# Optimization experiments

Measured on AMD Instinct MI355X. Metric: run time of the kernel, lower is better.

The kernel has to match this reference:

```python
import jax, jax.numpy as jnp
import numpy as np

B, S, HID, NH = 4, 2048, 512, 8
DH = HID // NH
NEG = -1000000.0


def setup_inputs() -> dict:
    key = jax.random.key(0)
    ks = jax.random.split(key, 8)
    scale = 1.0 / np.sqrt(HID)
    return {
        "queries": jax.random.normal(ks[0], (B, S, HID), dtype=jnp.float32),
        "keys": jax.random.normal(ks[1], (B, S, HID), dtype=jnp.float32),
        "values": jax.random.normal(ks[2], (B, S, HID), dtype=jnp.float32),
        "valid_lens": jax.random.randint(ks[3], (B,), 1, S + 1, dtype=jnp.int32),
        "Wq": jax.random.uniform(ks[4], (HID, HID), jnp.float32, -scale, scale),
        "Wk": jax.random.uniform(ks[5], (HID, HID), jnp.float32, -scale, scale),
        "Wv": jax.random.uniform(ks[6], (HID, HID), jnp.float32, -scale, scale),
        "Wo": jax.random.uniform(ks[7], (HID, HID), jnp.float32, -scale, scale),
    }


def _split_heads(x):
    # (B, S, HID) -> (B, NH, S, DH)
    return x.reshape(B, S, NH, DH).transpose(0, 2, 1, 3)


def reference(queries, keys, values, valid_lens, Wq, Wk, Wv, Wo):
    q = _split_heads(queries @ Wq.T)
    k = _split_heads(keys @ Wk.T)
    v = _split_heads(values @ Wv.T)
    scores = jnp.einsum("bhqd,bhkd->bhqk", q, k) / jnp.sqrt(jnp.float32(DH))
    # valid_lens is per-batch; mask key positions >= valid_len with -1e6 (as in sequence_mask)
    mask = jnp.arange(S)[None, :] < valid_lens[:, None]          # (B, S)
    scores = jnp.where(mask[:, None, None, :], scores, NEG)
    attn = jax.nn.softmax(scores, axis=-1)
    out = jnp.einsum("bhqk,bhkd->bhqd", attn, v)                 # (B, NH, S, DH)
    out = out.transpose(0, 2, 1, 3).reshape(B, S, HID)
    return out @ Wo.T
```

## Files before the change

### kernel.cpp

```cpp
#include <hip/hip_runtime.h>

#define B_ 4
#define S_ 2048
#define HIDN 512
#define NH 8
#define DH 64

typedef __attribute__((ext_vector_type(8))) short short8;
typedef __attribute__((ext_vector_type(4))) short short4v;
typedef __attribute__((ext_vector_type(8))) __bf16 bf16x8;
typedef __attribute__((ext_vector_type(4))) float floatx4;
typedef __attribute__((ext_vector_type(2))) unsigned uint2v;
typedef __attribute__((ext_vector_type(4))) unsigned uint4v;

__device__ inline short f2bf(float f) {
    union { float f; unsigned u; } x; x.f = f;
    unsigned r = x.u + 0x7fffu + ((x.u >> 16) & 1u);
    return (short)(r >> 16);
}

__device__ inline unsigned pack2(float a, float b) {
    unsigned ua = __builtin_bit_cast(unsigned, a) + 0x8000u;
    unsigned ub = __builtin_bit_cast(unsigned, b) + 0x8000u;
    return __builtin_amdgcn_perm(ub, ua, 0x07060302);
}

__device__ inline short8 cvt8(const float* __restrict__ p) {
    floatx4 f0 = *(const floatx4*)p;
    floatx4 f1 = *(const floatx4*)(p + 4);
    uint4v u;
    u[0] = pack2(f0[0], f0[1]); u[1] = pack2(f0[2], f0[3]);
    u[2] = pack2(f1[0], f1[1]); u[3] = pack2(f1[2], f1[3]);
    return __builtin_bit_cast(short8, u);
}

__device__ inline floatx4 mfma_s(short8 a, short8 b, floatx4 c) {
    return __builtin_amdgcn_mfma_f32_16x16x32_bf16(
        __builtin_bit_cast(bf16x8, a), __builtin_bit_cast(bf16x8, b), c, 0, 0, 0);
}

__device__ inline float vmax4(floatx4 v) {
    return fmaxf(fmaxf(v[0], v[1]), fmaxf(v[2], v[3]));
}

__device__ inline void gl_lds(const short* g, short* l) {
    __builtin_amdgcn_global_load_lds(
        (const __attribute__((address_space(1))) void*)g,
        (__attribute__((address_space(3))) void*)l, 16, 0, 0);
}

__global__ void cvt_w(const float* __restrict__ wq, const float* __restrict__ wk,
                      const float* __restrict__ wv, short* __restrict__ out) {
    const float* src = blockIdx.y == 0 ? wq : (blockIdx.y == 1 ? wk : wv);
    int i = (blockIdx.x * 256 + threadIdx.x) * 4;
    floatx4 f = *(const floatx4*)&src[i];
    short4v v; v[0]=f2bf(f[0]); v[1]=f2bf(f[1]); v[2]=f2bf(f[2]); v[3]=f2bf(f[3]);
    *(short4v*)&out[blockIdx.y * (HIDN * HIDN) + i] = v;
}

__global__ __launch_bounds__(256) void gemm_qkv(const float* __restrict__ xq,
                                                const float* __restrict__ xk,
                                                const float* __restrict__ xv,
                                                const short* __restrict__ wb,
                                                short* __restrict__ Qh,
                                                short* __restrict__ Kh,
                                                short* __restrict__ VT) {
    const int z = blockIdx.z;
    const float* X = z == 0 ? xq : (z == 1 ? xk : xv);
    const short* W = wb + z * (HIDN * HIDN);
    short* dstQK = z == 0 ? Qh : Kh;

    __shared__ __align__(16) short Als[128][72];
    __shared__ __align__(16) short Bls[128][72];

    const int t = threadIdx.x;
    const int w = t >> 6, lane = t & 63, quad = lane >> 4, l16 = lane & 15;
    const int wm = (w & 1) * 64, wn = (w >> 1) * 64;
    const int m0 = blockIdx.x * 128, n0 = blockIdx.y * 128;

    floatx4 acc[4][4];
    floatx4 zero = {0.f, 0.f, 0.f, 0.f};
#pragma unroll
    for (int i = 0; i < 4; i++)
#pragma unroll
        for (int j = 0; j < 4; j++) acc[i][j] = zero;

    const int row0 = t >> 3;
    const int c8 = (t & 7) * 8;

    for (int k0 = 0; k0 < HIDN; k0 += 64) {
        __syncthreads();
#pragma unroll
        for (int rr = 0; rr < 4; rr++)
            *(short8*)&Als[row0 + rr*32][c8] =
                cvt8(&X[(m0 + row0 + rr*32) * HIDN + k0 + c8]);
#pragma unroll
        for (int rr = 0; rr < 4; rr++)
            *(short8*)&Bls[row0 + rr*32][c8] =
                *(const short8*)&W[(n0 + row0 + rr*32) * HIDN + k0 + c8];
        __syncthreads();

#pragma unroll
        for (int ks = 0; ks < 2; ks++) {
            const int cq8 = (ks * 4 + quad) * 8;
            short8 a[4], b[4];
#pragma unroll
            for (int i = 0; i < 4; i++)
                a[i] = *(const short8*)&Als[wm + i*16 + l16][cq8];
#pragma unroll
            for (int j = 0; j < 4; j++)
                b[j] = *(const short8*)&Bls[wn + j*16 + l16][cq8];
#pragma unroll
            for (int i = 0; i < 4; i++)
#pragma unroll
                for (int j = 0; j < 4; j++)
                    acc[i][j] = mfma_s(a[i], b[j], acc[i][j]);
        }
    }

    if (z < 2) {
#pragma unroll
        for (int i = 0; i < 4; i++)
#pragma unroll
            for (int j = 0; j < 4; j++)
#pragma unroll
                for (int r = 0; r < 4; r++) {
                    int m = m0 + wm + i*16 + quad*4 + r;
                    int n = n0 + wn + j*16 + l16;
                    int bb = m >> 11, s = m & 2047, h = n >> 6, d = n & 63;
                    dstQK[((bb * NH + h) * S_ + s) * DH + d] = f2bf(acc[i][j][r]);
                }
    } else {
#pragma unroll
        for (int i = 0; i < 4; i++)
#pragma unroll
            for (int j = 0; j < 4; j++) {
                int s0 = m0 + wm + i*16 + quad*4;
                int n = n0 + wn + j*16 + l16;
                int bb = s0 >> 11, s = s0 & 2047, h = n >> 6, d = n & 63;
                uint2v v;
                v[0] = pack2(acc[i][j][0], acc[i][j][1]);
                v[1] = pack2(acc[i][j][2], acc[i][j][3]);
                *(uint2v*)&VT[((bb * NH + h) * DH + d) * S_ + s] = v;
            }
    }
}

__global__ __launch_bounds__(256) void gemm_out(const short* __restrict__ AO,
                                                const float* __restrict__ Wo,
                                                float* __restrict__ C) {
    __shared__ __align__(16) short Als[128][72];
    __shared__ __align__(16) short Bls[64][72];

    const int t = threadIdx.x;
    const int w = t >> 6, lane = t & 63, quad = lane >> 4, l16 = lane & 15;
    const int wm = (w & 1) * 64, wn = (w >> 1) * 32;
    const int m0 = blockIdx.x * 128, n0 = blockIdx.y * 64;

    floatx4 acc[4][2];
    floatx4 zero = {0.f, 0.f, 0.f, 0.f};
#pragma unroll
    for (int i = 0; i < 4; i++)
#pragma unroll
        for (int j = 0; j < 2; j++) acc[i][j] = zero;

    const int row0 = t >> 3;
    const int c8 = (t & 7) * 8;

    for (int k0 = 0; k0 < HIDN; k0 += 64) {
        __syncthreads();
#pragma unroll
        for (int rr = 0; rr < 4; rr++)
            *(short8*)&Als[row0 + rr*32][c8] =
                *(const short8*)&AO[(m0 + row0 + rr*32) * HIDN + k0 + c8];
#pragma unroll
        for (int rr = 0; rr < 2; rr++)
            *(short8*)&Bls[row0 + rr*32][c8] =
                cvt8(&Wo[(n0 + row0 + rr*32) * HIDN + k0 + c8]);
        __syncthreads();

#pragma unroll
        for (int ks = 0; ks < 2; ks++) {
            const int cq8 = (ks * 4 + quad) * 8;
            short8 a[4], b[2];
#pragma unroll
            for (int i = 0; i < 4; i++)
                a[i] = *(const short8*)&Als[wm + i*16 + l16][cq8];
#pragma unroll
            for (int j = 0; j < 2; j++)
                b[j] = *(const short8*)&Bls[wn + j*16 + l16][cq8];
#pragma unroll
            for (int i = 0; i < 4; i++)
#pragma unroll
                for (int j = 0; j < 2; j++)
                    acc[i][j] = mfma_s(a[i], b[j], acc[i][j]);
        }
    }

#pragma unroll
    for (int i = 0; i < 4; i++)
#pragma unroll
        for (int j = 0; j < 2; j++)
#pragma unroll
            for (int r = 0; r < 4; r++) {
                int m = m0 + wm + i*16 + quad*4 + r;
                int n = n0 + wn + j*16 + l16;
                C[m * HIDN + n] = acc[i][j][r];
            }
}

__global__ __launch_bounds__(256, 2) void attn_kernel(const short* __restrict__ Qh,
                                                      const short* __restrict__ Kh,
                                                      const short* __restrict__ VT,
                                                      const int* __restrict__ vlen,
                                                      short* __restrict__ AO) {
    __shared__ __align__(16) short Ksh[2][128 * 64];
    __shared__ __align__(16) short Vsh[2][64 * 128];

    const int t = threadIdx.x, w = t >> 6, lane = t & 63;
    const int quad = lane >> 4, l16 = lane & 15;
    const int qb = blockIdx.x * 64;
    const int h = blockIdx.y, b = blockIdx.z;
    const int bh = b * NH + h;
    const int vl = vlen[b];
    const int nt = (vl + 127) >> 7;

    const float SC = 0.180336879f;

    const short* qrow = &Qh[(bh * S_ + qb + w * 16 + l16) * DH];
    short8 qa0 = *(const short8*)&qrow[quad * 8];
    short8 qa1 = *(const short8*)&qrow[32 + quad * 8];

    int kgo[4], vgo[4];
#pragma unroll
    for (int it = 0; it < 4; it++) {
        int idx = it * 256 + t;
        int row = idx >> 3, c = idx & 7;
        kgo[it] = row * DH + ((c ^ (row & 7)) << 3);
        int d = idx >> 4, cv = idx & 15;
        vgo[it] = d * S_ + ((cv ^ (d & 7)) << 3);
    }
    const int ldsb = (t & ~63) * 8;

    const short* Kgb = &Kh[(size_t)bh * S_ * DH];
    const short* Vgb = &VT[(size_t)bh * DH * S_];

#define STAGE(bufsel, tb)                                                     \
    {                                                                         \
        const short* Kg_ = Kgb + (tb) * DH;                                   \
        const short* Vg_ = Vgb + (tb);                                        \
        _Pragma("unroll")                                                     \
        for (int it = 0; it < 4; it++)                                        \
            gl_lds(Kg_ + kgo[it], &Ksh[bufsel][it * 2048 + ldsb]);            \
        _Pragma("unroll")                                                     \
        for (int it = 0; it < 4; it++)                                        \
            gl_lds(Vg_ + vgo[it], &Vsh[bufsel][it * 2048 + ldsb]);            \
    }

    STAGE(0, 0)

    float m_run = -1e30f, l_run = 0.f;
    floatx4 Oacc[4];
    floatx4 zero = {0.f, 0.f, 0.f, 0.f};
#pragma unroll
    for (int dt = 0; dt < 4; dt++) Oacc[dt] = zero;

    for (int kt = 0; kt < nt; kt++) {
        const int base = kt << 7;
        const bool bnd = (base + 128) > vl;
        const int cur = kt & 1;
        const short* Kc = Ksh[cur];
        const short* Vc = Vsh[cur];
        short* Psh = Ksh[cur];

        __syncthreads();

        if (kt + 1 < nt) STAGE(cur ^ 1, base + 128)

        floatx4 sc[8];
#pragma unroll
        for (int n = 0; n < 8; n++) {
            int kro = n * 16 + l16;
            const short* kr = &Kc[kro * 64];
            short8 kb0 = *(const short8*)&kr[((quad ^ (kro & 7)) << 3)];
            short8 kb1 = *(const short8*)&kr[(((4 + quad) ^ (kro & 7)) << 3)];
            floatx4 s = zero;
            s = mfma_s(kb0, qa0, s);
            s = mfma_s(kb1, qa1, s);
            sc[n] = s;
        }
        __syncthreads();

        if (bnd) {
#pragma unroll
            for (int n = 0; n < 8; n++)
#pragma unroll
                for (int r = 0; r < 4; r++) {
                    int key = base + n * 16 + quad * 4 + r;
                    if (key >= vl) sc[n][r] = -1e30f;
                }
        }

        float mx = vmax4(sc[0]);
#pragma unroll
        for (int n = 1; n < 8; n++) mx = fmaxf(mx, vmax4(sc[n]));
        mx = fmaxf(mx, __shfl_xor(mx, 16));
        mx = fmaxf(mx, __shfl_xor(mx, 32));
        const float mxs = mx * SC;
        const bool norescale = __all(mxs <= m_run);
        const float mnew = norescale ? m_run : fmaxf(m_run, mxs);
        const float alpha = norescale ? 1.0f : __builtin_amdgcn_exp2f(m_run - mnew);
        m_run = mnew;
        float rs = 0.f;
#pragma unroll
        for (int n = 0; n < 8; n++)
#pragma unroll
            for (int r = 0; r < 4; r++) {
                float p = __builtin_amdgcn_exp2f(fmaf(sc[n][r], SC, -mnew));
                sc[n][r] = p;
                rs += p;
            }
        rs += __shfl_xor(rs, 16);
        rs += __shfl_xor(rs, 32);
        l_run = l_run * alpha + rs;
        if (!norescale) {
#pragma unroll
            for (int dt = 0; dt < 4; dt++)
#pragma unroll
                for (int r = 0; r < 4; r++) Oacc[dt][r] *= alpha;
        }

#pragma unroll
        for (int n = 0; n < 8; n++) {
            unsigned lo = pack2(sc[n][0], sc[n][1]);
            unsigned hi = pack2(sc[n][2], sc[n][3]);
            int c = (n << 1) + (quad >> 1);
            int idx = (w << 11) + (l16 << 7) + ((c ^ (l16 & 7)) << 3) + ((quad & 1) << 2);
            uint2v pv; pv[0] = lo; pv[1] = hi;
            *(uint2v*)&Psh[idx] = pv;
        }
        asm volatile("s_waitcnt lgkmcnt(0)" ::: "memory");
        __builtin_amdgcn_sched_barrier(0);

#pragma unroll
        for (int kk = 0; kk < 4; kk++) {
            int pc = (kk << 2) + quad;
            short8 pf = *(const short8*)&Psh[(w << 11) + (l16 << 7) + ((pc ^ (l16 & 7)) << 3)];
#pragma unroll
            for (int dt = 0; dt < 4; dt++) {
                int vrow = dt * 16 + l16;
                short8 vf = *(const short8*)&Vc[vrow * 128 + ((pc ^ (vrow & 7)) << 3)];
                Oacc[dt] = mfma_s(vf, pf, Oacc[dt]);
            }
        }
    }
#undef STAGE

    float inv = 1.0f / l_run;
    int q = qb + w * 16 + l16;
    short* dst = &AO[(b * S_ + q) * HIDN + h * DH];
#pragma unroll
    for (int dt = 0; dt < 4; dt++) {
        uint2v v;
        v[0] = pack2(Oacc[dt][0] * inv, Oacc[dt][1] * inv);
        v[1] = pack2(Oacc[dt][2] * inv, Oacc[dt][3] * inv);
        *(uint2v*)&dst[dt * 16 + quad * 4] = v;
    }
}

extern "C" void kernel_launch(void* const* d_in, const int* in_sizes, int n_in,
                              void* d_out, int out_size, void* d_ws, size_t ws_size,
                              hipStream_t stream) {
    const float* q  = (const float*)d_in[0];
    const float* k  = (const float*)d_in[1];
    const float* v  = (const float*)d_in[2];
    const int*   vl = (const int*)d_in[3];
    const float* wq = (const float*)d_in[4];
    const float* wk = (const float*)d_in[5];
    const float* wv = (const float*)d_in[6];
    const float* wo = (const float*)d_in[7];
    float* out = (float*)d_out;

    const size_t HSZ = (size_t)B_ * NH * S_ * DH;
    short* Qh  = (short*)d_ws;
    short* Kh  = Qh + HSZ;
    short* VT  = Kh + HSZ;
    short* AO  = VT + HSZ;
    short* Wqkv = AO;

    dim3 blk(256);
    cvt_w<<<dim3(256, 3), blk, 0, stream>>>(wq, wk, wv, Wqkv);
    gemm_qkv<<<dim3(64, 4, 3), blk, 0, stream>>>(q, k, v, Wqkv, Qh, Kh, VT);
    attn_kernel<<<dim3(S_ / 64, NH, B_), blk, 0, stream>>>(Qh, Kh, VT, vl, AO);
    gemm_out<<<dim3(64, 8), blk, 0, stream>>>(AO, wo, out);
}
```

Measured before the change: 189.4 us.

## Split attention KV loop across two warp groups with in-block softmax merge

The attention block grows to 512 threads, split into two 256-thread groups. Each group handles alternating 128-key tiles for the same 64 queries, and at the end the two partial softmax states (max, sum, output) are merged through LDS. The async global-to-LDS double-buffered prefetch is replaced by synchronous register loads into one buffer per group, so tile loads no longer overlap compute. The aim is to halve the serial KV loop per block and raise wave-level parallelism, at the cost of losing load/compute overlap, adding extra barriers and a merge step, and using more registers per CU.

```diff
diff --git a/kernel.cpp b/kernel.cpp
--- a/kernel.cpp
+++ b/kernel.cpp
@@ -41,12 +41,6 @@
 
 __device__ inline float vmax4(floatx4 v) {
     return fmaxf(fmaxf(v[0], v[1]), fmaxf(v[2], v[3]));
-}
-
-__device__ inline void gl_lds(const short* g, short* l) {
-    __builtin_amdgcn_global_load_lds(
-        (const __attribute__((address_space(1))) void*)g,
-        (__attribute__((address_space(3))) void*)l, 16, 0, 0);
 }
 
 __global__ void cvt_w(const float* __restrict__ wq, const float* __restrict__ wk,
@@ -209,7 +203,7 @@
             }
 }
 
-__global__ __launch_bounds__(256, 2) void attn_kernel(const short* __restrict__ Qh,
+__global__ __launch_bounds__(512, 4) void attn_kernel(const short* __restrict__ Qh,
                                                       const short* __restrict__ Kh,
                                                       const short* __restrict__ VT,
                                                       const int* __restrict__ vlen,
@@ -217,13 +211,17 @@
     __shared__ __align__(16) short Ksh[2][128 * 64];
     __shared__ __align__(16) short Vsh[2][64 * 128];
 
-    const int t = threadIdx.x, w = t >> 6, lane = t & 63;
-    const int quad = lane >> 4, l16 = lane & 15;
+    const int t = threadIdx.x;
+    const int g = t >> 8;
+    const int tg = t & 255;
+    const int w = (t >> 6) & 3;
+    const int lane = t & 63, quad = lane >> 4, l16 = lane & 15;
     const int qb = blockIdx.x * 64;
     const int h = blockIdx.y, b = blockIdx.z;
     const int bh = b * NH + h;
     const int vl = vlen[b];
     const int nt = (vl + 127) >> 7;
+    const int nrounds = (nt + 1) >> 1;
 
     const float SC = 0.180336879f;
 
@@ -231,33 +229,9 @@
     short8 qa0 = *(const short8*)&qrow[quad * 8];
     short8 qa1 = *(const short8*)&qrow[32 + quad * 8];
 
-    int kgo[4], vgo[4];
-#pragma unroll
-    for (int it = 0; it < 4; it++) {
-        int idx = it * 256 + t;
-        int row = idx >> 3, c = idx & 7;
-        kgo[it] = row * DH + ((c ^ (row & 7)) << 3);
-        int d = idx >> 4, cv = idx & 15;
-        vgo[it] = d * S_ + ((cv ^ (d & 7)) << 3);
-    }
-    const int ldsb = (t & ~63) * 8;
-
-    const short* Kgb = &Kh[(size_t)bh * S_ * DH];
-    const short* Vgb = &VT[(size_t)bh * DH * S_];
-
-#define STAGE(bufsel, tb)                                                     \
-    {                                                                         \
-        const short* Kg_ = Kgb + (tb) * DH;                                   \
-        const short* Vg_ = Vgb + (tb);                                        \
-        _Pragma("unroll")                                                     \
-        for (int it = 0; it < 4; it++)                                        \
-            gl_lds(Kg_ + kgo[it], &Ksh[bufsel][it * 2048 + ldsb]);            \
-        _Pragma("unroll")                                                     \
-        for (int it = 0; it < 4; it++)                                        \
-            gl_lds(Vg_ + vgo[it], &Vsh[bufsel][it * 2048 + ldsb]);            \
-    }
-
-    STAGE(0, 0)
+    short* Kc = Ksh[g];
+    short* Vc = Vsh[g];
+    short* Psh = Kc + (w << 11);
 
     float m_run = -1e30f, l_run = 0.f;
     floatx4 Oacc[4];
@@ -265,106 +239,146 @@
 #pragma unroll
     for (int dt = 0; dt < 4; dt++) Oacc[dt] = zero;
 
-    for (int kt = 0; kt < nt; kt++) {
+    for (int i = 0; i < nrounds; i++) {
+        const int kt = 2 * i + g;
+        const bool act = kt < nt;
         const int base = kt << 7;
         const bool bnd = (base + 128) > vl;
-        const int cur = kt & 1;
-        const short* Kc = Ksh[cur];
-        const short* Vc = Vsh[cur];
-        short* Psh = Ksh[cur];
-
-        __syncthreads();
-
-        if (kt + 1 < nt) STAGE(cur ^ 1, base + 128)
+
+        __syncthreads();
+        if (act) {
+            const short* Kg = &Kh[(bh * S_ + base) * DH];
+#pragma unroll
+            for (int it = 0; it < 4; it++) {
+                int idx = it * 256 + tg;
+                int row = idx >> 3, c = idx & 7;
+                *(short8*)&Kc[row * 64 + (((c ^ (row & 7))) << 3)] =
+                    *(const short8*)&Kg[row * DH + (c << 3)];
+            }
+            const short* Vg = &VT[bh * DH * S_ + base];
+#pragma unroll
+            for (int it = 0; it < 4; it++) {
+                int idx = it * 256 + tg;
+                int d = idx >> 4, c = idx & 15;
+                *(short8*)&Vc[d * 128 + (((c ^ (d & 7))) << 3)] =
+                    *(const short8*)&Vg[d * S_ + (c << 3)];
+            }
+        }
+        __syncthreads();
 
         floatx4 sc[8];
-#pragma unroll
-        for (int n = 0; n < 8; n++) {
-            int kro = n * 16 + l16;
-            const short* kr = &Kc[kro * 64];
-            short8 kb0 = *(const short8*)&kr[((quad ^ (kro & 7)) << 3)];
-            short8 kb1 = *(const short8*)&kr[(((4 + quad) ^ (kro & 7)) << 3)];
-            floatx4 s = zero;
-            s = mfma_s(kb0, qa0, s);
-            s = mfma_s(kb1, qa1, s);
-            sc[n] = s;
-        }
-        __syncthreads();
-
-        if (bnd) {
+        if (act) {
+#pragma unroll
+            for (int n = 0; n < 8; n++) {
+                int kro = n * 16 + l16;
+                const short* kr = &Kc[kro * 64];
+                short8 kb0 = *(const short8*)&kr[((quad ^ (kro & 7)) << 3)];
+                short8 kb1 = *(const short8*)&kr[(((4 + quad) ^ (kro & 7)) << 3)];
+                floatx4 s = zero;
+                s = mfma_s(kb0, qa0, s);
+                s = mfma_s(kb1, qa1, s);
+                sc[n] = s;
+            }
+        }
+        __syncthreads();
+
+        if (act) {
+            if (bnd) {
+#pragma unroll
+                for (int n = 0; n < 8; n++)
+#pragma unroll
+                    for (int r = 0; r < 4; r++) {
+                        int key = base + n * 16 + quad * 4 + r;
+                        if (key >= vl) sc[n][r] = -1e30f;
+                    }
+            }
+
+            float mx = vmax4(sc[0]);
+#pragma unroll
+            for (int n = 1; n < 8; n++) mx = fmaxf(mx, vmax4(sc[n]));
+            mx = fmaxf(mx, __shfl_xor(mx, 16));
+            mx = fmaxf(mx, __shfl_xor(mx, 32));
+            const float mxs = mx * SC;
+            const bool norescale = __all(mxs <= m_run);
+            const float mnew = norescale ? m_run : fmaxf(m_run, mxs);
+            const float alpha = norescale ? 1.0f : __builtin_amdgcn_exp2f(m_run - mnew);
+            m_run = mnew;
+            float rs = 0.f;
 #pragma unroll
             for (int n = 0; n < 8; n++)
 #pragma unroll
                 for (int r = 0; r < 4; r++) {
-                    int key = base + n * 16 + quad * 4 + r;
-                    if (key >= vl) sc[n][r] = -1e30f;
+                    float p = __builtin_amdgcn_exp2f(fmaf(sc[n][r], SC, -mnew));
+                    sc[n][r] = p;
+                    rs += p;
                 }
-        }
-
-        float mx = vmax4(sc[0]);
-#pragma unroll
-        for (int n = 1; n < 8; n++) mx = fmaxf(mx, vmax4(sc[n]));
-        mx = fmaxf(mx, __shfl_xor(mx, 16));
-        mx = fmaxf(mx, __shfl_xor(mx, 32));
-        const float mxs = mx * SC;
-        const bool norescale = __all(mxs <= m_run);
-        const float mnew = norescale ? m_run : fmaxf(m_run, mxs);
-        const float alpha = norescale ? 1.0f : __builtin_amdgcn_exp2f(m_run - mnew);
-        m_run = mnew;
-        float rs = 0.f;
-#pragma unroll
-        for (int n = 0; n < 8; n++)
-#pragma unroll
-            for (int r = 0; r < 4; r++) {
-                float p = __builtin_amdgcn_exp2f(fmaf(sc[n][r], SC, -mnew));
-                sc[n][r] = p;
-                rs += p;
-            }
-        rs += __shfl_xor(rs, 16);
-        rs += __shfl_xor(rs, 32);
-        l_run = l_run * alpha + rs;
-        if (!norescale) {
-#pragma unroll
-            for (int dt = 0; dt < 4; dt++)
-#pragma unroll
-                for (int r = 0; r < 4; r++) Oacc[dt][r] *= alpha;
-        }
-
-#pragma unroll
-        for (int n = 0; n < 8; n++) {
-            unsigned lo = pack2(sc[n][0], sc[n][1]);
-            unsigned hi = pack2(sc[n][2], sc[n][3]);
-            int c = (n << 1) + (quad >> 1);
-            int idx = (w << 11) + (l16 << 7) + ((c ^ (l16 & 7)) << 3) + ((quad & 1) << 2);
-            uint2v pv; pv[0] = lo; pv[1] = hi;
-            *(uint2v*)&Psh[idx] = pv;
-        }
-        asm volatile("s_waitcnt lgkmcnt(0)" ::: "memory");
-        __builtin_amdgcn_sched_barrier(0);
-
-#pragma unroll
-        for (int kk = 0; kk < 4; kk++) {
-            int pc = (kk << 2) + quad;
-            short8 pf = *(const short8*)&Psh[(w << 11) + (l16 << 7) + ((pc ^ (l16 & 7)) << 3)];
-#pragma unroll
-            for (int dt = 0; dt < 4; dt++) {
-                int vrow = dt * 16 + l16;
-                short8 vf = *(const short8*)&Vc[vrow * 128 + ((pc ^ (vrow & 7)) << 3)];
-                Oacc[dt] = mfma_s(vf, pf, Oacc[dt]);
-            }
-        }
-    }
-#undef STAGE
-
-    float inv = 1.0f / l_run;
-    int q = qb + w * 16 + l16;
-    short* dst = &AO[(b * S_ + q) * HIDN + h * DH];
-#pragma unroll
-    for (int dt = 0; dt < 4; dt++) {
-        uint2v v;
-        v[0] = pack2(Oacc[dt][0] * inv, Oacc[dt][1] * inv);
-        v[1] = pack2(Oacc[dt][2] * inv, Oacc[dt][3] * inv);
-        *(uint2v*)&dst[dt * 16 + quad * 4] = v;
+            rs += __shfl_xor(rs, 16);
+            rs += __shfl_xor(rs, 32);
+            l_run = l_run * alpha + rs;
+            if (!norescale) {
+#pragma unroll
+                for (int dt = 0; dt < 4; dt++)
+#pragma unroll
+                    for (int r = 0; r < 4; r++) Oacc[dt][r] *= alpha;
+            }
+
+#pragma unroll
+            for (int n = 0; n < 8; n++) {
+                unsigned lo = pack2(sc[n][0], sc[n][1]);
+                unsigned hi = pack2(sc[n][2], sc[n][3]);
+                int c = (n << 1) + (quad >> 1);
+                int idx = (l16 << 7) + ((c ^ (l16 & 7)) << 3) + ((quad & 1) << 2);
+                uint2v pv; pv[0] = lo; pv[1] = hi;
+                *(uint2v*)&Psh[idx] = pv;
+            }
+            asm volatile("s_waitcnt lgkmcnt(0)" ::: "memory");
+            __builtin_amdgcn_sched_barrier(0);
+
+#pragma unroll
+            for (int kk = 0; kk < 4; kk++) {
+                int pc = (kk << 2) + quad;
+                short8 pf = *(const short8*)&Psh[(l16 << 7) + ((pc ^ (l16 & 7)) << 3)];
+#pragma unroll
+                for (int dt = 0; dt < 4; dt++) {
+                    int vrow = dt * 16 + l16;
+                    short8 vf = *(const short8*)&Vc[vrow * 128 + ((pc ^ (vrow & 7)) << 3)];
+                    Oacc[dt] = mfma_s(vf, pf, Oacc[dt]);
+                }
+            }
+        }
+    }
+
+    __syncthreads();
+    float* Of = (float*)Ksh;
+    float* ml = (float*)Vsh;
+    if (g == 1) {
+#pragma unroll
+        for (int dt = 0; dt < 4; dt++) *(floatx4*)&Of[tg * 16 + dt * 4] = Oacc[dt];
+        ml[tg * 2] = m_run;
+        ml[tg * 2 + 1] = l_run;
+    }
+    __syncthreads();
+    if (g == 0) {
+        float m1 = ml[tg * 2], l1 = ml[tg * 2 + 1];
+        float mstar = fmaxf(m_run, m1);
+        float s0 = __builtin_amdgcn_exp2f(m_run - mstar);
+        float s1 = __builtin_amdgcn_exp2f(m1 - mstar);
+        float inv = 1.0f / (l_run * s0 + l1 * s1);
+        float a0 = s0 * inv, a1 = s1 * inv;
+        int q = qb + w * 16 + l16;
+        short* dst = &AO[(b * S_ + q) * HIDN + h * DH];
+#pragma unroll
+        for (int dt = 0; dt < 4; dt++) {
+            floatx4 o1 = *(const floatx4*)&Of[tg * 16 + dt * 4];
+            float v0 = Oacc[dt][0] * a0 + o1[0] * a1;
+            float v1 = Oacc[dt][1] * a0 + o1[1] * a1;
+            float v2 = Oacc[dt][2] * a0 + o1[2] * a1;
+            float v3 = Oacc[dt][3] * a0 + o1[3] * a1;
+            uint2v v;
+            v[0] = pack2(v0, v1);
+            v[1] = pack2(v2, v3);
+            *(uint2v*)&dst[dt * 16 + quad * 4] = v;
+        }
     }
 }
 
@@ -391,6 +405,6 @@
     dim3 blk(256);
     cvt_w<<<dim3(256, 3), blk, 0, stream>>>(wq, wk, wv, Wqkv);
     gemm_qkv<<<dim3(64, 4, 3), blk, 0, stream>>>(q, k, v, Wqkv, Qh, Kh, VT);
-    attn_kernel<<<dim3(S_ / 64, NH, B_), blk, 0, stream>>>(Qh, Kh, VT, vl, AO);
+    attn_kernel<<<dim3(S_ / 64, NH, B_), dim3(512), 0, stream>>>(Qh, Kh, VT, vl, AO);
     gemm_out<<<dim3(64, 8), blk, 0, stream>>>(AO, wo, out);
 }
```

Result: slower. 195.2 us (+3.1%).
